# Performance work log

Hardware: AMD Instinct MI355X
Metric: run time of the kernel (lower is better)

## Reference

```python
import jax, jax.numpy as jnp
import numpy as np

V, E, H = 32000, 512, 512
B, T = 64, 512


def lstm_dir(x, W, U, b, reverse=False):
    """Keras-semantics LSTM over [B,T,D] -> (hs [B,T,H], h_last, c_last).
    Gate order i,f,g,o; sigmoid recurrent activation, tanh activation.
    Inference mode: dropout=0.1 is inactive (Keras applies it only in training)."""
    xz = jnp.einsum('btd,dg->btg', x, W) + b  # precompute input projections [B,T,4H]
    if reverse:
        xz = xz[:, ::-1]
    h0 = jnp.zeros((x.shape[0], U.shape[0]), x.dtype)
    c0 = jnp.zeros_like(h0)

    def step(carry, zt):
        h, c = carry
        z = zt + h @ U
        i, f, g, o = jnp.split(z, 4, axis=-1)
        c = jax.nn.sigmoid(f) * c + jax.nn.sigmoid(i) * jnp.tanh(g)
        h = jax.nn.sigmoid(o) * jnp.tanh(c)
        return (h, c), h

    (h_last, c_last), hs = jax.lax.scan(step, (h0, c0), jnp.swapaxes(xz, 0, 1))
    hs = jnp.swapaxes(hs, 0, 1)  # [B,T,H]
    if reverse:
        hs = hs[:, ::-1]  # Keras Bidirectional re-aligns backward outputs in time
    return hs, h_last, c_last


def setup_inputs() -> dict:
    key = jax.random.key(0)
    ks = jax.random.split(key, 14)
    s = lambda fan_in: 1.0 / np.sqrt(fan_in)
    p = {
        'encoderinput': jax.random.randint(ks[0], (B, T), 0, V, dtype=jnp.int32),
        'emb': jax.random.normal(ks[1], (V, E), jnp.float32) * 0.02,
        # layer 1 (input dim E), forward and backward directions
        'W1f': jax.random.normal(ks[2], (E, 4 * H), jnp.float32) * s(E),
        'U1f': jax.random.normal(ks[3], (H, 4 * H), jnp.float32) * s(H),
        'b1f': jnp.zeros((4 * H,), jnp.float32),
        'W1b': jax.random.normal(ks[4], (E, 4 * H), jnp.float32) * s(E),
        'U1b': jax.random.normal(ks[5], (H, 4 * H), jnp.float32) * s(H),
        'b1b': jnp.zeros((4 * H,), jnp.float32),
        # layer 2 (input dim 2H from bidirectional concat)
        'W2f': jax.random.normal(ks[6], (2 * H, 4 * H), jnp.float32) * s(2 * H),
        'U2f': jax.random.normal(ks[7], (H, 4 * H), jnp.float32) * s(H),
        'b2f': jnp.zeros((4 * H,), jnp.float32),
        'W2b': jax.random.normal(ks[8], (2 * H, 4 * H), jnp.float32) * s(2 * H),
        'U2b': jax.random.normal(ks[9], (H, 4 * H), jnp.float32) * s(H),
        'b2b': jnp.zeros((4 * H,), jnp.float32),
    }
    return p


def reference(encoderinput, emb, W1f, U1f, b1f, W1b, U1b, b1b,
              W2f, U2f, b2f, W2b, U2b, b2b):
    x = emb[encoderinput]  # [B,T,E]
    hf1, _, _ = lstm_dir(x, W1f, U1f, b1f, reverse=False)
    hb1, _, _ = lstm_dir(x, W1b, U1b, b1b, reverse=True)
    l1 = jnp.concatenate([hf1, hb1], axis=-1)  # [B,T,2H]
    hf2, fh, fc = lstm_dir(l1, W2f, U2f, b2f, reverse=False)
    hb2, bh, bc = lstm_dir(l1, W2b, U2b, b2b, reverse=True)
    encoder_output = jnp.concatenate([hf2, hb2], axis=-1)  # [B,T,2H]
    state_h = jnp.concatenate([fh, bh], axis=-1)  # [B,2H]
    state_c = jnp.concatenate([fc, bc], axis=-1)  # [B,2H]
    return (encoder_output, state_h, state_c)
```

## Files before the change

### kernel.cpp

```cpp
#include <hip/hip_runtime.h>
#include <math.h>


#define NBLK_LSTM 256

typedef __attribute__((ext_vector_type(8))) short bf16x8;
typedef __attribute__((ext_vector_type(16))) float f32x16;

__device__ __forceinline__ float bf2f(unsigned short u) {
  return __uint_as_float(((unsigned)u) << 16);
}
__device__ __forceinline__ unsigned short f2bf(float f) {
  unsigned u = __float_as_uint(f);
  unsigned r = (u + 0x7FFFu + ((u >> 16) & 1u)) >> 16;
  return (unsigned short)r;
}
__device__ __forceinline__ float fsigmoid(float x) {
  return 1.0f / (1.0f + __expf(-x));
}
__device__ __forceinline__ float ftanh(float x) {
  return 1.0f - 2.0f / (1.0f + __expf(2.0f * x));
}
__device__ __forceinline__ void gload16(const void* g, void* l) {
  __builtin_amdgcn_global_load_lds(
      (const __attribute__((address_space(1))) unsigned int*)g,
      (__attribute__((address_space(3))) unsigned int*)l, 16, 0, 0);
}

__global__ __launch_bounds__(256) void transpose_u(const float* __restrict__ U,
                                                   float* __restrict__ Ut) {
  __shared__ float tile[32][33];
  int kt = blockIdx.x & 15;
  int ct = blockIdx.x >> 4;
  int k0 = kt * 32, c0 = ct * 32;
  int tx = threadIdx.x & 31, ty = threadIdx.x >> 5;
#pragma unroll
  for (int i = 0; i < 32; i += 8)
    tile[ty + i][tx] = U[(size_t)(k0 + ty + i) * 2048 + c0 + tx];
  __syncthreads();
#pragma unroll
  for (int i = 0; i < 32; i += 8)
    Ut[(size_t)(c0 + ty + i) * 512 + k0 + tx] = tile[tx][ty + i];
}

__global__ __launch_bounds__(256) void build_w_panels(
    const float* __restrict__ W, unsigned short* __restrict__ Wh,
    unsigned short* __restrict__ Wl, int KT) {
  __shared__ float tile[32][33];
  const int tid = threadIdx.x;
  int kt = blockIdx.x % KT;
  int ct = blockIdx.x / KT;
  int k0 = kt * 32, c0 = ct * 32;
  int tx = tid & 31, ty = tid >> 5;
#pragma unroll
  for (int i = 0; i < 32; i += 8)
    tile[ty + i][tx] = W[(size_t)(k0 + ty + i) * 2048 + c0 + tx];
  __syncthreads();
  const int t = tid & 127;
  const int cl = t & 31, g = t >> 5;
  const int c = c0 + cl;
  const int rm = c & 127, nt = c >> 7;
  const int slot = g ^ (rm & 3);
  size_t off = (((size_t)(nt * KT + kt) * 128 + rm) << 5) + slot * 8;
  bf16x8 hh, ll;
#pragma unroll
  for (int e = 0; e < 8; e++) {
    float f = tile[g * 8 + e][cl];
    unsigned short h = f2bf(f);
    hh[e] = (short)h;
    ll[e] = (short)f2bf(f - bf2f(h));
  }
  if (tid < 128) *(bf16x8*)(Wh + off) = hh;
  else           *(bf16x8*)(Wl + off) = ll;
}

__global__ __launch_bounds__(256) void build_a1_panels(
    const int* __restrict__ ids, const float* __restrict__ emb,
    unsigned short* __restrict__ Apan) {
  const int tid = threadIdx.x;
  const int l = tid & 63, wv = tid >> 6;
  const int m = blockIdx.x * 4 + wv;
  const float* src = emb + (size_t)ids[m] * 512 + l * 8;
  float4 v0 = *(const float4*)src;
  float4 v1 = *(const float4*)(src + 4);
  float f[8] = {v0.x, v0.y, v0.z, v0.w, v1.x, v1.y, v1.z, v1.w};
  bf16x8 hh;
#pragma unroll
  for (int e = 0; e < 8; e++) hh[e] = (short)f2bf(f[e]);
  const int rm = m & 127, mt = m >> 7;
  const int kt = l >> 2, g = l & 3;
  const int slot = g ^ (rm & 3);
  *(bf16x8*)(Apan + (((size_t)(mt * 16 + kt) * 128 + rm) << 5) + slot * 8) = hh;
}

template <int KT>
__global__ __launch_bounds__(256) void gemm_panel(
    const unsigned short* __restrict__ Apan,
    const unsigned short* __restrict__ WhP,
    const unsigned short* __restrict__ WlP,
    const float* __restrict__ bias,
    unsigned short* __restrict__ C) {
  __shared__ __align__(16) char lds[2][24576];

  const int tid = threadIdx.x;
  const int mt = blockIdx.x & 255;
  const int nt = blockIdx.x >> 8;
  const int l = tid & 63;
  const int wv = tid >> 6;
  const int wm = wv >> 1, wn = wv & 1;

  const char* aSrc = (const char*)(Apan + (size_t)mt * KT * 4096);
  const char* hSrc = (const char*)(WhP + (size_t)nt * KT * 4096);
  const char* lSrc = (const char*)(WlP + (size_t)nt * KT * 4096);
  const int wvo = wv * 1024;
  const int lo16 = l * 16;

  f32x16 acc[2][2];
#pragma unroll
  for (int rb = 0; rb < 2; rb++)
#pragma unroll
    for (int cb = 0; cb < 2; cb++)
#pragma unroll
      for (int r = 0; r < 16; r++) acc[rb][cb][r] = 0.0f;

  auto STAGE = [&](int buf, int t) {
    const char* ga = aSrc + (size_t)t * 8192 + wvo + lo16;
    const char* gh = hSrc + (size_t)t * 8192 + wvo + lo16;
    const char* gl = lSrc + (size_t)t * 8192 + wvo + lo16;
    char* da = &lds[buf][0] + wvo;
    char* dh = &lds[buf][8192] + wvo;
    char* dl = &lds[buf][16384] + wvo;
    gload16(ga, da);
    gload16(ga + 4096, da + 4096);
    gload16(gh, dh);
    gload16(gh + 4096, dh + 4096);
    gload16(gl, dl);
    gload16(gl + 4096, dl + 4096);
  };

  STAGE(0, 0);
  asm volatile("s_waitcnt vmcnt(0)" ::: "memory");
  __syncthreads();

  const int aoff0 = (wm * 64 + (l & 31)) * 64;
  const int woff0 = 8192 + (wn * 64 + (l & 31)) * 64;
  const int gbase = l >> 5;
  const int gx = l & 3;

  for (int t = 0; t < KT; t++) {
    if (t + 1 < KT) STAGE((t + 1) & 1, t + 1);
    const char* lb = lds[t & 1];
#pragma unroll
    for (int ks = 0; ks < 2; ks++) {
      const int slot = (((ks << 1) + gbase) ^ gx) << 4;
      bf16x8 a0 = *(const bf16x8*)(lb + aoff0 + slot);
      bf16x8 a1 = *(const bf16x8*)(lb + aoff0 + 2048 + slot);
      bf16x8 h0 = *(const bf16x8*)(lb + woff0 + slot);
      bf16x8 h1 = *(const bf16x8*)(lb + woff0 + 2048 + slot);
      bf16x8 w0 = *(const bf16x8*)(lb + woff0 + 8192 + slot);
      bf16x8 w1 = *(const bf16x8*)(lb + woff0 + 8192 + 2048 + slot);
      acc[0][0] = __builtin_amdgcn_mfma_f32_32x32x16_bf16(a0, h0, acc[0][0], 0, 0, 0);
      acc[0][1] = __builtin_amdgcn_mfma_f32_32x32x16_bf16(a0, h1, acc[0][1], 0, 0, 0);
      acc[1][0] = __builtin_amdgcn_mfma_f32_32x32x16_bf16(a1, h0, acc[1][0], 0, 0, 0);
      acc[1][1] = __builtin_amdgcn_mfma_f32_32x32x16_bf16(a1, h1, acc[1][1], 0, 0, 0);
      acc[0][0] = __builtin_amdgcn_mfma_f32_32x32x16_bf16(a0, w0, acc[0][0], 0, 0, 0);
      acc[0][1] = __builtin_amdgcn_mfma_f32_32x32x16_bf16(a0, w1, acc[0][1], 0, 0, 0);
      acc[1][0] = __builtin_amdgcn_mfma_f32_32x32x16_bf16(a1, w0, acc[1][0], 0, 0, 0);
      acc[1][1] = __builtin_amdgcn_mfma_f32_32x32x16_bf16(a1, w1, acc[1][1], 0, 0, 0);
    }
    asm volatile("s_waitcnt vmcnt(0)" ::: "memory");
    __syncthreads();
  }

  const int m0 = mt * 128, n0 = nt * 128;
  const float b0 = bias[n0 + wn * 64 + (l & 31)];
  const float b1 = bias[n0 + wn * 64 + 32 + (l & 31)];
#pragma unroll
  for (int rb = 0; rb < 2; rb++) {
    const int rowb = m0 + wm * 64 + rb * 32 + 4 * (l >> 5);
#pragma unroll
    for (int cb = 0; cb < 2; cb++) {
      const int col = n0 + wn * 64 + cb * 32 + (l & 31);
      const float bb = cb ? b1 : b0;
#pragma unroll
      for (int r = 0; r < 16; r++) {
        const int row = rowb + (r & 3) + 8 * (r >> 2);
        C[(size_t)row * 2048 + col] = f2bf(acc[rb][cb][r] + bb);
      }
    }
  }
}

__global__ __launch_bounds__(256, 1) void lstm_fused(
    const unsigned short* __restrict__ xzF,
    const unsigned short* __restrict__ xzB,
    const float* __restrict__ UtF,
    const float* __restrict__ UtB,
    float* __restrict__ outF32,
    unsigned short* __restrict__ outB16,
    float* __restrict__ hbuf,
    float* __restrict__ stateh, float* __restrict__ statec,
    unsigned* __restrict__ bar) {
  __shared__ __align__(16) char h_lds[65536];
  __shared__ float p_lds[4][32][36];

  const int tid = threadIdx.x;
  const int bid = blockIdx.x;
  const int dir = bid >> 7;
  const int jg  = (bid & 127) >> 1;
  const int bg  = bid & 1;
  const int grp = dir * 2 + bg;

  const unsigned short* xz = dir ? xzB : xzF;
  const float* Ut = dir ? UtB : UtF;
  char* hbuf_c = (char*)hbuf;

  const int l  = tid & 63;
  const int wv = tid >> 6;

  bf16x8 uh8[8], ul8[8];
  {
    const int c = l & 31;
    const size_t gcol = (size_t)((c >> 3) * 512 + jg * 8 + (c & 7));
#pragma unroll
    for (int ks = 0; ks < 8; ks++) {
      const float* src = Ut + gcol * 512 + (wv * 8 + ks) * 16 + ((l >> 5) << 3);
      bf16x8 hh, ll;
#pragma unroll
      for (int e = 0; e < 8; e++) {
        float f = src[e];
        unsigned short us = f2bf(f);
        hh[e] = (short)us;
        ll[e] = (short)f2bf(f - bf2f(us));
      }
      uh8[ks] = hh;
      ul8[ks] = ll;
    }
  }

  const int ub = tid >> 3;
  const int jl = tid & 7;
  const int b  = bg * 32 + ub;
  const int j  = jg * 8 + jl;

  unsigned* leafArr = bar + grp * 128;
  unsigned* myleaf  = leafArr + (jg & 7) * 16;

  const unsigned short* xzb = xz + (size_t)b * (512 * 2048) + j;

  float creg = 0.0f;
  float zx0, zx1, zx2, zx3;
  {
    const unsigned short* p = xzb + (size_t)(dir ? 511 : 0) * 2048;
    zx0 = bf2f(p[0]); zx1 = bf2f(p[512]);
    zx2 = bf2f(p[1024]); zx3 = bf2f(p[1536]);
  }

  const char* hrow = h_lds + (l & 31) * 1024;
  const int axr = (l & 7) << 4;
  const int koff = (l >> 5) << 4;
  const int hswz_w = (ub & 7) << 4;

  const int colp = dir * 512 + j;
  const int p_kt = colp >> 5, p_g = (colp >> 3) & 3, p_e = colp & 7;

  for (int s = 0; s < 512; s++) {
    const int tt = dir ? (511 - s) : s;

    if (s > 0) {
      const char* sb = hbuf_c + (size_t)(grp * 2 + (s & 1)) * 65536;
      float4 hv[16];
#pragma unroll
      for (int i = 0; i < 16; i++) {
        const float* p = (const float*)(sb + (size_t)(i * 256 + tid) * 16);
        asm volatile("global_load_dwordx4 %0, %1, off sc0 sc1"
                     : "=v"(hv[i]) : "v"(p) : "memory");
      }
      asm volatile("s_waitcnt vmcnt(0)" ::: "memory");
      __builtin_amdgcn_sched_barrier(0);
#pragma unroll
      for (int i = 0; i < 16; i++)
        *(float4*)(h_lds + (size_t)(i * 256 + tid) * 16) = hv[i];
    }
    __syncthreads();

    if (s > 0) {
      f32x16 acc;
#pragma unroll
      for (int r = 0; r < 16; r++) acc[r] = 0.0f;
#pragma unroll
      for (int ks = 0; ks < 8; ks++) {
        const int boff = (((wv * 8 + ks) << 5) + koff) ^ axr;
        bf16x8 ahh = *(const bf16x8*)(hrow + boff);
        bf16x8 ahl = *(const bf16x8*)(hrow + 32768 + boff);
        acc = __builtin_amdgcn_mfma_f32_32x32x16_bf16(ahh, uh8[ks], acc, 0, 0, 0);
        acc = __builtin_amdgcn_mfma_f32_32x32x16_bf16(ahl, uh8[ks], acc, 0, 0, 0);
        acc = __builtin_amdgcn_mfma_f32_32x32x16_bf16(ahh, ul8[ks], acc, 0, 0, 0);
      }
#pragma unroll
      for (int r = 0; r < 16; r++) {
        const int row = (r & 3) + 8 * (r >> 2) + 4 * (l >> 5);
        p_lds[wv][row][l & 31] = acc[r];
      }
    }
    __syncthreads();

    float h;
    {
      float z0 = zx0, z1 = zx1, z2 = zx2, z3 = zx3;
      if (s > 0) {
#pragma unroll
        for (int w = 0; w < 4; w++) {
          z0 += p_lds[w][ub][jl];
          z1 += p_lds[w][ub][8 + jl];
          z2 += p_lds[w][ub][16 + jl];
          z3 += p_lds[w][ub][24 + jl];
        }
      }
      float si = fsigmoid(z0);
      float sf = fsigmoid(z1);
      float tg = ftanh(z2);
      float so = fsigmoid(z3);
      creg = fmaf(sf, creg, si * tg);
      h = so * ftanh(creg);
    }

    const int m = b * 512 + tt;
    if (s < 511) {
      unsigned short hhs = f2bf(h);
      unsigned short hls = f2bf(h - bf2f(hhs));
      char* db = hbuf_c + (size_t)(grp * 2 + ((s & 1) ^ 1)) * 65536;
      char* pj = db + ub * 1024 + ((j * 2) ^ hswz_w);
      unsigned vh = hhs, vl = hls;
      asm volatile("global_store_short %0, %1, off sc0 sc1"
                   :: "v"(pj), "v"(vh) : "memory");
      asm volatile("global_store_short %0, %1, off sc0 sc1"
                   :: "v"(pj + 32768), "v"(vl) : "memory");
      asm volatile("s_waitcnt vmcnt(0)" ::: "memory");
      __syncthreads();
      if (tid == 0)
        __hip_atomic_fetch_add(myleaf, 1u, __ATOMIC_RELAXED,
                               __HIP_MEMORY_SCOPE_AGENT);
      if (outB16) {
        const int rm = m & 127, mt = m >> 7;
        outB16[(((size_t)(mt * 32 + p_kt) * 128 + rm) << 5) +
               (p_g ^ (rm & 3)) * 8 + p_e] = f2bf(h);
      } else {
        outF32[((size_t)m) * 1024 + colp] = h;
      }
      {
        const int tn = dir ? (510 - s) : (s + 1);
        const unsigned short* p = xzb + (size_t)tn * 2048;
        zx0 = bf2f(p[0]); zx1 = bf2f(p[512]);
        zx2 = bf2f(p[1024]); zx3 = bf2f(p[1536]);
      }
      if (tid < 8) {
        const unsigned tgt = 8u * (unsigned)(s + 1);
        while (__hip_atomic_load(leafArr + tid * 16, __ATOMIC_RELAXED,
                                 __HIP_MEMORY_SCOPE_AGENT) < tgt)
          __builtin_amdgcn_s_sleep(1);
      }
      __syncthreads();
    } else {
      if (outB16) {
        const int rm = m & 127, mt = m >> 7;
        outB16[(((size_t)(mt * 32 + p_kt) * 128 + rm) << 5) +
               (p_g ^ (rm & 3)) * 8 + p_e] = f2bf(h);
      } else {
        outF32[((size_t)m) * 1024 + colp] = h;
      }
      if (stateh != nullptr) {
        stateh[b * 1024 + colp] = h;
        statec[b * 1024 + colp] = creg;
      }
    }
  }
}

extern "C" void kernel_launch(void* const* d_in, const int* in_sizes, int n_in,
                              void* d_out, int out_size, void* d_ws, size_t ws_size,
                              hipStream_t stream) {
  const int*   ids = (const int*)d_in[0];
  const float* emb = (const float*)d_in[1];
  const float* W1f = (const float*)d_in[2];
  const float* U1f = (const float*)d_in[3];
  const float* b1f = (const float*)d_in[4];
  const float* W1b = (const float*)d_in[5];
  const float* U1b = (const float*)d_in[6];
  const float* b1b = (const float*)d_in[7];
  const float* W2f = (const float*)d_in[8];
  const float* U2f = (const float*)d_in[9];
  const float* b2f = (const float*)d_in[10];
  const float* W2b = (const float*)d_in[11];
  const float* U2b = (const float*)d_in[12];
  const float* b2b = (const float*)d_in[13];
  float* out = (float*)d_out;

  char* ws = (char*)d_ws;
  unsigned short* xzF = (unsigned short*)(ws + 0ull);
  unsigned short* xzB = (unsigned short*)(ws + 134217728ull);
  float* Ut1f = (float*)(ws + 268435456ull);
  float* Ut1b = Ut1f + 1048576;
  float* Ut2f = Ut1b + 1048576;
  float* Ut2b = Ut2f + 1048576;
  float* hbuf = (float*)(ws + 285212672ull);
  unsigned* bar = (unsigned*)(ws + 285736960ull);

  char* outc = (char*)d_out;
  unsigned short* l1pan = (unsigned short*)outc;
  unsigned short* A1pan = (unsigned short*)(outc + 67108864ull);
  unsigned short* Wh1f = (unsigned short*)(outc + 100663296ull);
  unsigned short* Wl1f = (unsigned short*)(outc + 102760448ull);
  unsigned short* Wh1b = (unsigned short*)(outc + 104857600ull);
  unsigned short* Wl1b = (unsigned short*)(outc + 106954752ull);
  unsigned short* Wh2f = (unsigned short*)(outc + 109051904ull);
  unsigned short* Wl2f = (unsigned short*)(outc + 113246208ull);
  unsigned short* Wh2b = (unsigned short*)(outc + 117440512ull);
  unsigned short* Wl2b = (unsigned short*)(outc + 121634816ull);

  transpose_u<<<1024, 256, 0, stream>>>(U1f, Ut1f);
  transpose_u<<<1024, 256, 0, stream>>>(U1b, Ut1b);
  transpose_u<<<1024, 256, 0, stream>>>(U2f, Ut2f);
  transpose_u<<<1024, 256, 0, stream>>>(U2b, Ut2b);
  build_w_panels<<<1024, 256, 0, stream>>>(W1f, Wh1f, Wl1f, 16);
  build_w_panels<<<1024, 256, 0, stream>>>(W1b, Wh1b, Wl1b, 16);
  build_w_panels<<<2048, 256, 0, stream>>>(W2f, Wh2f, Wl2f, 32);
  build_w_panels<<<2048, 256, 0, stream>>>(W2b, Wh2b, Wl2b, 32);
  build_a1_panels<<<8192, 256, 0, stream>>>(ids, emb, A1pan);

  gemm_panel<16><<<4096, 256, 0, stream>>>(A1pan, Wh1f, Wl1f, b1f, xzF);
  gemm_panel<16><<<4096, 256, 0, stream>>>(A1pan, Wh1b, Wl1b, b1b, xzB);
  hipMemsetAsync(bar, 0, 4096, stream);
  lstm_fused<<<NBLK_LSTM, 256, 0, stream>>>(xzF, xzB, Ut1f, Ut1b,
                                            nullptr, l1pan, hbuf,
                                            nullptr, nullptr, bar);
  gemm_panel<32><<<4096, 256, 0, stream>>>(l1pan, Wh2f, Wl2f, b2f, xzF);
  gemm_panel<32><<<4096, 256, 0, stream>>>(l1pan, Wh2b, Wl2b, b2b, xzB);
  hipMemsetAsync(bar, 0, 4096, stream);
  lstm_fused<<<NBLK_LSTM, 256, 0, stream>>>(xzF, xzB, Ut2f, Ut2b,
                                            out, nullptr, hbuf,
                                            out + 33554432, out + 33619968, bar);
}
```

Baseline: 4.992 ms.

## Load MFMA A-fragments of h directly from global in fragment-major layout

Each step's h exchange buffer is now written in an MFMA-fragment-major layout, so each wave loads its A operands (hi and lo bf16 parts) straight from global memory into registers. This removes the 64KB LDS staging buffer, the LDS store/load round trip and one __syncthreads per timestep on the serial recurrence. In exchange each block issues 16 dwordx4 loads per thread of partly redundant data, and the layout of hbuf writes changes.

```diff
diff --git a/kernel.cpp b/kernel.cpp
--- a/kernel.cpp
+++ b/kernel.cpp
@@ -201,7 +201,6 @@
     float* __restrict__ hbuf,
     float* __restrict__ stateh, float* __restrict__ statec,
     unsigned* __restrict__ bar) {
-  __shared__ __align__(16) char h_lds[65536];
   __shared__ float p_lds[4][32][36];
 
   const int tid = threadIdx.x;
@@ -256,10 +255,8 @@
     zx2 = bf2f(p[1024]); zx3 = bf2f(p[1536]);
   }
 
-  const char* hrow = h_lds + (l & 31) * 1024;
-  const int axr = (l & 7) << 4;
-  const int koff = (l >> 5) << 4;
-  const int hswz_w = (ub & 7) << 4;
+  const int aoff = ((wv * 16 + (l >> 5)) * 32 + (l & 31)) * 16;
+  const int poff = jg * 512 + ub * 16 + jl * 2;
 
   const int colp = dir * 512 + j;
   const int p_kt = colp >> 5, p_g = (colp >> 3) & 3, p_e = colp & 7;
@@ -269,33 +266,26 @@
 
     if (s > 0) {
       const char* sb = hbuf_c + (size_t)(grp * 2 + (s & 1)) * 65536;
-      float4 hv[16];
-#pragma unroll
-      for (int i = 0; i < 16; i++) {
-        const float* p = (const float*)(sb + (size_t)(i * 256 + tid) * 16);
+      bf16x8 ahh[8], ahl[8];
+#pragma unroll
+      for (int ks = 0; ks < 8; ks++) {
+        const char* p = sb + aoff + ks * 1024;
         asm volatile("global_load_dwordx4 %0, %1, off sc0 sc1"
-                     : "=v"(hv[i]) : "v"(p) : "memory");
+                     : "=v"(ahh[ks]) : "v"(p) : "memory");
+        asm volatile("global_load_dwordx4 %0, %1, off sc0 sc1"
+                     : "=v"(ahl[ks]) : "v"(p + 32768) : "memory");
       }
       asm volatile("s_waitcnt vmcnt(0)" ::: "memory");
       __builtin_amdgcn_sched_barrier(0);
-#pragma unroll
-      for (int i = 0; i < 16; i++)
-        *(float4*)(h_lds + (size_t)(i * 256 + tid) * 16) = hv[i];
-    }
-    __syncthreads();
-
-    if (s > 0) {
+
       f32x16 acc;
 #pragma unroll
       for (int r = 0; r < 16; r++) acc[r] = 0.0f;
 #pragma unroll
       for (int ks = 0; ks < 8; ks++) {
-        const int boff = (((wv * 8 + ks) << 5) + koff) ^ axr;
-        bf16x8 ahh = *(const bf16x8*)(hrow + boff);
-        bf16x8 ahl = *(const bf16x8*)(hrow + 32768 + boff);
-        acc = __builtin_amdgcn_mfma_f32_32x32x16_bf16(ahh, uh8[ks], acc, 0, 0, 0);
-        acc = __builtin_amdgcn_mfma_f32_32x32x16_bf16(ahl, uh8[ks], acc, 0, 0, 0);
-        acc = __builtin_amdgcn_mfma_f32_32x32x16_bf16(ahh, ul8[ks], acc, 0, 0, 0);
+        acc = __builtin_amdgcn_mfma_f32_32x32x16_bf16(ahh[ks], uh8[ks], acc, 0, 0, 0);
+        acc = __builtin_amdgcn_mfma_f32_32x32x16_bf16(ahl[ks], uh8[ks], acc, 0, 0, 0);
+        acc = __builtin_amdgcn_mfma_f32_32x32x16_bf16(ahh[ks], ul8[ks], acc, 0, 0, 0);
       }
 #pragma unroll
       for (int r = 0; r < 16; r++) {
@@ -330,7 +320,7 @@
       unsigned short hhs = f2bf(h);
       unsigned short hls = f2bf(h - bf2f(hhs));
       char* db = hbuf_c + (size_t)(grp * 2 + ((s & 1) ^ 1)) * 65536;
-      char* pj = db + ub * 1024 + ((j * 2) ^ hswz_w);
+      char* pj = db + poff;
       unsigned vh = hhs, vl = hls;
       asm volatile("global_store_short %0, %1, off sc0 sc1"
                    :: "v"(pj), "v"(vh) : "memory");
```

Measured after the change: 4.731 ms. 1.06x faster.
